# Optimization experiments

Measured on AMD Instinct MI355X. Metric: run time of the kernel, lower is better.

## Reference

```python
import jax, jax.numpy as jnp
import numpy as np

N_LAYERS = 4
D_MODEL = 64        # 8*8 hardcoded in source
D_STATE = 128
D_CONV = 4
EXPAND = 2
HEADDIM = 64        # Mamba2Simple default
D_INNER = EXPAND * D_MODEL            # 128
NHEADS = D_INNER // HEADDIM           # 2
NGROUPS = 1
D_IN_PROJ = 2 * D_INNER + 2 * NGROUPS * D_STATE + NHEADS   # 514
CONV_DIM = D_INNER + 2 * NGROUPS * D_STATE                 # 384
EPS = 1e-5
B_SZ, SEQ = 8, 4096


def setup_inputs() -> dict:
    key = jax.random.key(0)
    ks = jax.random.split(key, 8)
    s = 0.02
    x = jax.random.normal(ks[0], (B_SZ, SEQ, D_MODEL), jnp.float32)
    in_proj_w = jax.random.normal(ks[1], (N_LAYERS, D_IN_PROJ, D_MODEL), jnp.float32) * s
    conv_w = jax.random.normal(ks[2], (N_LAYERS, CONV_DIM, 1, D_CONV), jnp.float32) * 0.2
    conv_b = jnp.zeros((N_LAYERS, CONV_DIM), jnp.float32)
    # dt_bias ~ inverse-softplus of small dt values
    dt_bias = jax.random.uniform(ks[3], (N_LAYERS, NHEADS), jnp.float32, -4.0, 0.0)
    A_log = jnp.log(jax.random.uniform(ks[4], (N_LAYERS, NHEADS), jnp.float32, 1.0, 16.0))
    D = jnp.ones((N_LAYERS, NHEADS), jnp.float32)
    norm_w = jnp.ones((N_LAYERS, D_INNER), jnp.float32)
    out_proj_w = jax.random.normal(ks[5], (N_LAYERS, D_MODEL, D_INNER), jnp.float32) * s
    return {"x": x, "in_proj_w": in_proj_w, "conv_w": conv_w, "conv_b": conv_b,
            "dt_bias": dt_bias, "A_log": A_log, "D": D, "norm_w": norm_w,
            "out_proj_w": out_proj_w}


def _ssm(xh, dt, A, Bm, Cm):
    """Selective-scan SSM. xh:(B,L,H,P) dt:(B,L,H) A:(H,) Bm,Cm:(B,L,S) -> (B,L,H,P)"""
    dA = jnp.exp(dt * A)  # (B,L,H)

    def step(h, inp):
        dA_t, dt_t, x_t, B_t, C_t = inp
        # h: (B,H,P,S)
        h = h * dA_t[:, :, None, None] + (dt_t[:, :, None] * x_t)[..., None] * B_t[:, None, None, :]
        y = jnp.einsum('bhps,bs->bhp', h, C_t)
        return h, y

    b = xh.shape[0]
    h0 = jnp.zeros((b, NHEADS, HEADDIM, D_STATE), xh.dtype)
    xs = (jnp.moveaxis(dA, 1, 0), jnp.moveaxis(dt, 1, 0), jnp.moveaxis(xh, 1, 0),
          jnp.moveaxis(Bm, 1, 0), jnp.moveaxis(Cm, 1, 0))
    _, ys = jax.lax.scan(step, h0, xs)
    return jnp.moveaxis(ys, 0, 1)


def _layer(x, p):
    in_w, cw, cb, dtb, Alog, Dp, nw, ow = p
    zxbcdt = x @ in_w.T                                   # (B,L,514)
    z = zxbcdt[..., :D_INNER]
    xBC = zxbcdt[..., D_INNER:D_INNER + CONV_DIM]
    dt = jax.nn.softplus(zxbcdt[..., -NHEADS:] + dtb)     # (B,L,H)
    # causal depthwise conv over sequence
    xc = jnp.moveaxis(xBC, -1, 1)                         # (B,C,L)
    xc = jax.lax.conv_general_dilated(xc, cw, (1,), [(D_CONV - 1, 0)],
                                      dimension_numbers=('NCH', 'OIH', 'NCH'),
                                      feature_group_count=CONV_DIM)
    xBC = jax.nn.silu(jnp.moveaxis(xc + cb[None, :, None], 1, -1))
    xs = xBC[..., :D_INNER]
    Bm = xBC[..., D_INNER:D_INNER + D_STATE]
    Cm = xBC[..., D_INNER + D_STATE:]
    xh = xs.reshape(xs.shape[0], xs.shape[1], NHEADS, HEADDIM)
    A = -jnp.exp(Alog)                                    # (H,)
    y = _ssm(xh, dt, A, Bm, Cm) + Dp[None, None, :, None] * xh
    y = y.reshape(y.shape[0], y.shape[1], D_INNER)
    # gated RMSNorm (norm_before_gate=False): rmsnorm(y * silu(z)) * w
    y = y * jax.nn.silu(z)
    y = y * jax.lax.rsqrt(jnp.mean(y * y, axis=-1, keepdims=True) + EPS) * nw
    return y @ ow.T


def reference(x, in_proj_w, conv_w, conv_b, dt_bias, A_log, D, norm_w, out_proj_w):
    def body(xc, p):
        return _layer(xc, p) + xc, None
    out, _ = jax.lax.scan(body, x, (in_proj_w, conv_w, conv_b, dt_bias, A_log, D, norm_w, out_proj_w))
    return out
```

## Files before the change

kernel.cpp:

```cpp
#include <hip/hip_runtime.h>
#include <math.h>

#define B_SZ 8
#define SEQ  4096
#define DM   64
#define DI   128
#define NH   2
#define HD   64
#define DS   128
#define DIP  514
#define XW   384
#define CD   384
#define QC   64
#define NC   64
#define NR   (B_SZ*SEQ)
#define WPAD 576

typedef __attribute__((ext_vector_type(8))) short bf16x8;
typedef __attribute__((ext_vector_type(4))) float f32x4;
typedef __attribute__((ext_vector_type(2))) __bf16 bf16x2;

__device__ __forceinline__ unsigned short f2bf(float f) {
    union { __bf16 h; unsigned short u; } x;
    x.h = (__bf16)f;
    return x.u;
}
__device__ __forceinline__ unsigned int pk2(float lo, float hi) {
    union { bf16x2 v; unsigned int u; } x;
    x.v[0] = (__bf16)lo;
    x.v[1] = (__bf16)hi;
    return x.u;
}
__device__ __forceinline__ float bf2f(unsigned short h) {
    union { unsigned int u; float f; } x; x.u = ((unsigned int)h) << 16;
    return x.f;
}
__device__ __forceinline__ bf16x8 fragld(const unsigned short* base, int r0, int k0, int ld) {
    int l = threadIdx.x & 63;
    return *(const bf16x8*)(base + (ptrdiff_t)(r0 + (l & 15)) * ld + k0 + (l >> 4) * 8);
}

__global__ __launch_bounds__(256) void k_wcvt(const float* __restrict__ in_w,
                                              const float* __restrict__ out_w,
                                              unsigned short* __restrict__ Wb,
                                              unsigned short* __restrict__ OWb) {
    int idx = blockIdx.x * 256 + threadIdx.x;
    if (idx < 4 * WPAD * 64) {
        int l = idx / (WPAD * 64), r = idx % (WPAD * 64);
        int n = r >> 6, k = r & 63;
        float v = (n < DIP) ? in_w[(size_t)l * DIP * 64 + (size_t)n * 64 + k] : 0.f;
        Wb[idx] = f2bf(v);
    }
    if (idx < 4 * 64 * 128) OWb[idx] = f2bf(out_w[idx]);
}

__global__ __launch_bounds__(256) void k_xcvt(const float* __restrict__ X,
                                              unsigned short* __restrict__ Xb) {
    int idx = (blockIdx.x * 256 + threadIdx.x) * 4;
    float4 v = *(const float4*)(X + idx);
    uint2 p;
    p.x = pk2(v.x, v.y);
    p.y = pk2(v.z, v.w);
    *(uint2*)(Xb + idx) = p;
}

__global__ __launch_bounds__(256) void k_inproj(const unsigned short* __restrict__ Xb,
                                                const unsigned short* __restrict__ Wb,
                                                unsigned short* __restrict__ ZXb,
                                                float* __restrict__ DT) {
    int m0 = blockIdx.x * 256;
    int ny = blockIdx.y;
    int tid = threadIdx.x;
    int wid = tid >> 6, lane = tid & 63;
    int q4 = lane >> 4, c16 = lane & 15;
    int mb = m0 + wid * 64;
    bf16x8 af[4][2];
#pragma unroll
    for (int mt = 0; mt < 4; mt++)
#pragma unroll
        for (int ks = 0; ks < 2; ks++)
            af[mt][ks] = *(const bf16x8*)(Xb + (size_t)(mb + mt * 16 + c16) * 64 + ks * 32 + q4 * 8);
    if (ny < 6) {
#pragma unroll
        for (int nt = 0; nt < 4; nt++) {
            bf16x8 bf[2];
#pragma unroll
            for (int ks = 0; ks < 2; ks++)
                bf[ks] = *(const bf16x8*)(Wb + (size_t)(128 + ny * 64 + nt * 16 + c16) * 64 + ks * 32 + q4 * 8);
#pragma unroll
            for (int mt = 0; mt < 4; mt++) {
                f32x4 acc = {0.f, 0.f, 0.f, 0.f};
                acc = __builtin_amdgcn_mfma_f32_16x16x32_bf16(af[mt][0], bf[0], acc, 0, 0, 0);
                acc = __builtin_amdgcn_mfma_f32_16x16x32_bf16(af[mt][1], bf[1], acc, 0, 0, 0);
#pragma unroll
                for (int rr = 0; rr < 4; rr++) {
                    float v = acc[rr];
                    float vn = __shfl_xor(v, 1);
                    if (!(lane & 1)) {
                        unsigned int pk = pk2(v, vn);
                        *(unsigned int*)(ZXb + (size_t)(mb + mt * 16 + q4 * 4 + rr) * XW + ny * 64 + nt * 16 + c16) = pk;
                    }
                }
            }
        }
    } else {
        bf16x8 bf[2];
#pragma unroll
        for (int ks = 0; ks < 2; ks++)
            bf[ks] = *(const bf16x8*)(Wb + (size_t)(512 + c16) * 64 + ks * 32 + q4 * 8);
#pragma unroll
        for (int mt = 0; mt < 4; mt++) {
            f32x4 acc = {0.f, 0.f, 0.f, 0.f};
            acc = __builtin_amdgcn_mfma_f32_16x16x32_bf16(af[mt][0], bf[0], acc, 0, 0, 0);
            acc = __builtin_amdgcn_mfma_f32_16x16x32_bf16(af[mt][1], bf[1], acc, 0, 0, 0);
            if (c16 < 2)
#pragma unroll
                for (int rr = 0; rr < 4; rr++)
                    DT[(size_t)(mb + mt * 16 + q4 * 4 + rr) * 2 + c16] = acc[rr];
        }
    }
}

__global__ __launch_bounds__(1024, 8) void k_chunk1(
        const unsigned short* __restrict__ ZXb, const float* __restrict__ DT,
        const float* __restrict__ CW, const float* __restrict__ CB,
        const float* __restrict__ dtb, const float* __restrict__ Alog,
        const float* __restrict__ Dv,
        unsigned short* __restrict__ SL, unsigned short* __restrict__ CBuf,
        float* __restrict__ EB,
        float* __restrict__ TB, unsigned short* __restrict__ YBb) {
    __shared__ unsigned short sBt[128][72];
    __shared__ unsigned short sXt[128][72];
    __shared__ unsigned short uBC[2][64][136];
    __shared__ float s_cum[2][64], s_dt[2][64], s_w[2][64];
    unsigned short (*sM)[64][72] = (unsigned short (*)[64][72])&uBC[0][0][0];

    int c = blockIdx.x, b = blockIdx.y;
    size_t rbase = (size_t)b * SEQ + c * QC;
    int tid = threadIdx.x;
    int wid = tid >> 6, lane = tid & 63;
    int q4 = lane >> 4, c16 = lane & 15;

    if (wid < 2) {
        int h = wid, j = lane;
        float raw = DT[(rbase + j) * 2 + h] + dtb[h];
        float dt = (raw > 20.f) ? raw : log1pf(__expf(raw));
        float A = -__expf(Alog[h]);
        float x = dt * A;
        for (int off = 1; off < 64; off <<= 1) {
            float o = __shfl_up(x, off);
            if (lane >= off) x += o;
        }
        float T = __shfl(x, 63);
        s_dt[h][j] = dt;
        s_cum[h][j] = x;
        s_w[h][j] = __expf(T - x) * dt;
        EB[((size_t)(b * NC + c)) * 128 + h * 64 + j] = __expf(x);
        if (j == 0) TB[(b * 2 + h) * NC + c] = __expf(T);
    }

    size_t cbbase = ((size_t)(b * NC + c)) * 8192;
    for (int e = tid; e < 64 * 96; e += 1024) {
        int j = e / 96;
        int q = e - j * 96;
        int cc = q * 4;
        int l = c * QC + j;
        const unsigned short* zp = ZXb + (rbase + j) * XW + cc;
        uint2 a0 = *(const uint2*)zp;
        uint2 a1 = make_uint2(0, 0), a2 = make_uint2(0, 0), a3 = make_uint2(0, 0);
        if (l >= 1) a1 = *(const uint2*)(zp - XW);
        if (l >= 2) a2 = *(const uint2*)(zp - 2 * XW);
        if (l >= 3) a3 = *(const uint2*)(zp - 3 * XW);
        float v[4];
#pragma unroll
        for (int u = 0; u < 4; u++) {
            unsigned int w0 = (u < 2) ? a0.x : a0.y;
            unsigned int w1 = (u < 2) ? a1.x : a1.y;
            unsigned int w2 = (u < 2) ? a2.x : a2.y;
            unsigned int w3 = (u < 2) ? a3.x : a3.y;
            int sh = (u & 1) * 16;
            float r0 = bf2f((unsigned short)(w0 >> sh));
            float r1 = bf2f((unsigned short)(w1 >> sh));
            float r2 = bf2f((unsigned short)(w2 >> sh));
            float r3 = bf2f((unsigned short)(w3 >> sh));
            float4 wv = *(const float4*)(CW + (cc + u) * 4);
            float tt = CB[cc + u] + wv.w * r0 + wv.z * r1 + wv.y * r2 + wv.x * r3;
            v[u] = tt / (1.f + __expf(-tt));
        }
        if (cc < 128) {
#pragma unroll
            for (int u = 0; u < 4; u++) sXt[cc + u][j] = f2bf(v[u]);
        } else if (cc < 256) {
            int s = cc - 128;
            unsigned int p0 = pk2(v[0], v[1]);
            unsigned int p1 = pk2(v[2], v[3]);
            *(uint2*)&uBC[0][j][s] = make_uint2(p0, p1);
#pragma unroll
            for (int u = 0; u < 4; u++) sBt[s + u][j] = f2bf(v[u]);
        } else {
            int s = cc - 256;
            unsigned int p0 = pk2(v[0], v[1]);
            unsigned int p1 = pk2(v[2], v[3]);
            *(uint2*)&uBC[1][j][s] = make_uint2(p0, p1);
            *(uint2*)(CBuf + cbbase + (size_t)j * 128 + s) = make_uint2(p0, p1);
        }
    }
    __syncthreads();

    f32x4 gacc;
    {
        int it = wid >> 2, jt = wid & 3;
        f32x4 acc = {0.f, 0.f, 0.f, 0.f};
        for (int ks = 0; ks < 4; ks++) {
            bf16x8 a = fragld(&uBC[1][0][0], it * 16, ks * 32, 136);
            bf16x8 bb = fragld(&uBC[0][0][0], jt * 16, ks * 32, 136);
            acc = __builtin_amdgcn_mfma_f32_16x16x32_bf16(a, bb, acc, 0, 0, 0);
        }
        gacc = acc;
    }
    __syncthreads();
    {
        int it = wid >> 2, jt = wid & 3;
        int j = jt * 16 + c16;
        for (int rr = 0; rr < 4; rr++) {
            int i = it * 16 + q4 * 4 + rr;
            float gv = gacc[rr];
            for (int h = 0; h < 2; h++) {
                float m = 0.f;
                if (j <= i) m = gv * __expf(s_cum[h][i] - s_cum[h][j]) * s_dt[h][j];
                sM[h][i][j] = f2bf(m);
            }
        }
    }
    __syncthreads();

    size_t ybase = ((size_t)(b * NC + c)) * 8192;
#pragma unroll
    for (int u = 0; u < 2; u++) {
        int idx = wid * 2 + u;
        int h = idx >> 4, tt = idx & 15;
        int it = tt >> 2, pt = tt & 3;
        float dco = Dv[h];
        int pg = h * 64 + pt * 16 + c16;
        f32x4 acc;
        for (int rr = 0; rr < 4; rr++) {
            int i = it * 16 + q4 * 4 + rr;
            acc[rr] = dco * bf2f(sXt[pg][i]);
        }
        for (int ks = 0; ks < 2; ks++) {
            bf16x8 a = fragld(&sM[h][0][0], it * 16, ks * 32, 72);
            bf16x8 bb = fragld(&sXt[0][0], h * 64 + pt * 16, ks * 32, 72);
            acc = __builtin_amdgcn_mfma_f32_16x16x32_bf16(a, bb, acc, 0, 0, 0);
        }
        uint2 pk;
        pk.x = pk2(acc[0], acc[1]);
        pk.y = pk2(acc[2], acc[3]);
        *(uint2*)(YBb + ybase + (size_t)idx * 256 + lane * 4) = pk;
    }
    __syncthreads();
    {
        int row = tid >> 3, c0 = (tid & 7) * 8;
        uint4 xv = *(uint4*)&sXt[row][c0];
        const float* wp = s_w[row >> 6];
        unsigned int* px = &xv.x;
        uint4 ov;
        unsigned int* po = &ov.x;
#pragma unroll
        for (int t = 0; t < 4; t++) {
            float lo = bf2f((unsigned short)(px[t] & 0xffff)) * wp[c0 + 2 * t];
            float hi = bf2f((unsigned short)(px[t] >> 16)) * wp[c0 + 2 * t + 1];
            po[t] = pk2(lo, hi);
        }
        *(uint4*)&sXt[row][c0] = ov;
    }
    __syncthreads();
    size_t slbase = ((size_t)(b * NC + c)) * 16384;
#pragma unroll
    for (int u = 0; u < 4; u++) {
        int idx = wid * 4 + u;
        int ptl = idx >> 3, st = idx & 7;
        f32x4 acc = {0.f, 0.f, 0.f, 0.f};
        for (int ks = 0; ks < 2; ks++) {
            bf16x8 a = fragld(&sXt[0][0], ptl * 16, ks * 32, 72);
            bf16x8 bb = fragld(&sBt[0][0], st * 16, ks * 32, 72);
            acc = __builtin_amdgcn_mfma_f32_16x16x32_bf16(a, bb, acc, 0, 0, 0);
        }
        int s = st * 16 + c16;
        for (int rr = 0; rr < 4; rr++) {
            int p = ptl * 16 + q4 * 4 + rr;
            float vv = acc[rr];
            float vn = __shfl_xor(vv, 1);
            if (!(lane & 1)) {
                unsigned int pk = pk2(vv, vn);
                *(unsigned int*)(SL + slbase + (size_t)p * 128 + s) = pk;
            }
        }
    }
}

__global__ __launch_bounds__(256) void k_scan(unsigned short* __restrict__ SL,
                                              const float* __restrict__ TB) {
    int bid = blockIdx.x;
    int b = bid >> 5;
    int pu = (bid & 31) * 256 + threadIdx.x;
    int h = pu >> 12;
    const float* dAp = TB + (b * 2 + h) * NC;
    size_t base = (size_t)(b * NC) * 16384 + (size_t)pu * 2;
    float h0 = 0.f, h1 = 0.f;
#pragma unroll 8
    for (int cc = 0; cc < NC; cc++) {
        size_t idx = base + (size_t)cc * 16384;
        unsigned int v = *(unsigned int*)(SL + idx);
        float s0 = bf2f((unsigned short)(v & 0xffff));
        float s1 = bf2f((unsigned short)(v >> 16));
        *(unsigned int*)(SL + idx) = pk2(h0, h1);
        float dA = dAp[cc];
        h0 = h0 * dA + s0;
        h1 = h1 * dA + s1;
    }
}

__global__ __launch_bounds__(1024, 8) void k_fused(
        const unsigned short* __restrict__ SL, const unsigned short* __restrict__ CBuf,
        const float* __restrict__ EB,
        const unsigned short* __restrict__ YBb, const unsigned short* __restrict__ Wzb,
        const float* __restrict__ NW, const unsigned short* __restrict__ OWb,
        unsigned short* __restrict__ Xb, float* __restrict__ OutF,
        const unsigned short* __restrict__ WbN,
        unsigned short* __restrict__ ZXbO,
        float* __restrict__ DTO,
        int last) {
    __shared__ __attribute__((aligned(16))) unsigned short sH[128][136];
    __shared__ __attribute__((aligned(16))) unsigned short sE[128][136];
    float* sGf = (float*)&sH[0][0];
    unsigned short (*sG)[136] = (unsigned short (*)[136])&sE[0][0];
    unsigned short (*sX2)[72] = (unsigned short (*)[72])&sH[0][0];

    int c = blockIdx.x, b = blockIdx.y;
    size_t rbase = (size_t)b * SEQ + c * QC;
    int tid = threadIdx.x;
    int wid = tid >> 6, lane = tid & 63;
    size_t base = ((size_t)(b * NC + c)) * 16384;
    for (int u = 0; u < 2; u++) {
        int e = u * 1024 + tid;
        int row = e >> 4, cb8 = (e & 15) * 8;
        *(uint4*)&sH[row][cb8] = *(const uint4*)(SL + base + (size_t)row * 128 + cb8);
    }
    size_t cbbase = ((size_t)(b * NC + c)) * 8192;
    size_t ebase  = ((size_t)(b * NC + c)) * 128;
    {
        int i = tid >> 4, sc = (tid & 15) * 8;
        uint4 cv = *(const uint4*)(CBuf + cbbase + (size_t)i * 128 + sc);
        float e0 = EB[ebase + i], e1 = EB[ebase + 64 + i];
        unsigned int w[4] = {cv.x, cv.y, cv.z, cv.w};
        uint4 o0, o1;
        unsigned int* po0 = &o0.x;
        unsigned int* po1 = &o1.x;
#pragma unroll
        for (int t = 0; t < 4; t++) {
            float lo = bf2f((unsigned short)(w[t] & 0xffff));
            float hi = bf2f((unsigned short)(w[t] >> 16));
            po0[t] = pk2(lo * e0, hi * e0);
            po1[t] = pk2(lo * e1, hi * e1);
        }
        *(uint4*)&sE[i][sc] = o0;
        *(uint4*)&sE[64 + i][sc] = o1;
    }
    __syncthreads();
    int q4 = lane >> 4, c16 = lane & 15;

    float yv[2][4];
    int tit[2], tpg[2];
    size_t ybase = ((size_t)(b * NC + c)) * 8192;
#pragma unroll
    for (int u = 0; u < 2; u++) {
        int idx = wid * 2 + u;
        int h = idx >> 4, tt = idx & 15;
        int it = tt >> 2, pt = tt & 3;
        int pg = h * 64 + pt * 16 + c16;
        f32x4 zacc = {0.f, 0.f, 0.f, 0.f};
        f32x4 acc = {0.f, 0.f, 0.f, 0.f};
#pragma unroll
        for (int ks = 0; ks < 2; ks++) {
            bf16x8 xa = fragld(Xb, (int)rbase + it * 16, ks * 32, 64);
            bf16x8 wz = fragld(Wzb, h * 64 + pt * 16, ks * 32, 64);
            zacc = __builtin_amdgcn_mfma_f32_16x16x32_bf16(xa, wz, zacc, 0, 0, 0);
        }
        for (int ks = 0; ks < 4; ks++) {
            bf16x8 a = fragld(&sE[0][0], h * 64 + it * 16, ks * 32, 136);
            bf16x8 bb = fragld(&sH[0][0], h * 64 + pt * 16, ks * 32, 136);
            acc = __builtin_amdgcn_mfma_f32_16x16x32_bf16(a, bb, acc, 0, 0, 0);
        }
        tit[u] = it; tpg[u] = pg;
        uint2 yi = *(const uint2*)(YBb + ybase + (size_t)idx * 256 + lane * 4);
        float yin[4] = {bf2f((unsigned short)(yi.x & 0xffff)), bf2f((unsigned short)(yi.x >> 16)),
                        bf2f((unsigned short)(yi.y & 0xffff)), bf2f((unsigned short)(yi.y >> 16))};
        for (int rr = 0; rr < 4; rr++) {
            float y = acc[rr] + yin[rr];
            float z = zacc[rr];
            yv[u][rr] = y * (z / (1.f + __expf(-z)));
        }
    }
    __syncthreads();
#pragma unroll
    for (int u = 0; u < 2; u++)
        for (int rr = 0; rr < 4; rr++) {
            int i = tit[u] * 16 + q4 * 4 + rr;
            sGf[i * 132 + tpg[u]] = yv[u][rr];
        }
    __syncthreads();
    {
        int row = tid >> 4, part = tid & 15;
        int d0 = part * 8;
        float g[8];
        float ss = 0.f;
        for (int t2 = 0; t2 < 8; t2++) { g[t2] = sGf[row * 132 + d0 + t2]; ss += g[t2] * g[t2]; }
        ss += __shfl_xor(ss, 1);
        ss += __shfl_xor(ss, 2);
        ss += __shfl_xor(ss, 4);
        ss += __shfl_xor(ss, 8);
        float rms = rsqrtf(ss * (1.f / 128.f) + 1e-5f);
        for (int t2 = 0; t2 < 8; t2 += 2) {
            unsigned int pk = pk2(g[t2] * rms * NW[d0 + t2], g[t2 + 1] * rms * NW[d0 + t2 + 1]);
            *(unsigned int*)&sG[row][d0 + t2] = pk;
        }
    }
    __syncthreads();
    {
        int mt = wid >> 2, nt = wid & 3;
        f32x4 acc = {0.f, 0.f, 0.f, 0.f};
        for (int ks = 0; ks < 4; ks++) {
            bf16x8 a = fragld(&sG[0][0], mt * 16, ks * 32, 136);
            bf16x8 bb = *(const bf16x8*)(OWb + (size_t)(nt * 16 + c16) * 128 + ks * 32 + q4 * 8);
            acc = __builtin_amdgcn_mfma_f32_16x16x32_bf16(a, bb, acc, 0, 0, 0);
        }
        for (int rr = 0; rr < 4; rr++) {
            int m = mt * 16 + q4 * 4 + rr;
            int n = nt * 16 + c16;
            size_t o = (rbase + m) * DM + n;
            float v = bf2f(Xb[o]) + acc[rr];
            if (last) {
                OutF[o] = v;
            } else {
                unsigned short vb = f2bf(v);
                sX2[m][n] = vb;
                float vn = __shfl_xor(v, 1);
                if (!(lane & 1)) {
                    unsigned int pk = (unsigned int)vb | ((unsigned int)f2bf(vn) << 16);
                    *(unsigned int*)(Xb + o) = pk;
                }
            }
        }
    }
    if (!last) {
        __syncthreads();
        for (int t = wid; t < 100; t += 16) {
            int mt2, n0;
            int isdt = (t >= 96);
            if (!isdt) { mt2 = t & 3; n0 = (t >> 2) * 16; }
            else       { mt2 = t - 96; n0 = 0; }
            bf16x8 a0 = fragld(&sX2[0][0], mt2 * 16, 0, 72);
            bf16x8 a1 = fragld(&sX2[0][0], mt2 * 16, 32, 72);
            const unsigned short* wrow = isdt ? (WbN + (size_t)(512 + c16) * 64)
                                              : (WbN + (size_t)(128 + n0 + c16) * 64);
            bf16x8 b0 = *(const bf16x8*)(wrow + q4 * 8);
            bf16x8 b1 = *(const bf16x8*)(wrow + 32 + q4 * 8);
            f32x4 acc = {0.f, 0.f, 0.f, 0.f};
            acc = __builtin_amdgcn_mfma_f32_16x16x32_bf16(a0, b0, acc, 0, 0, 0);
            acc = __builtin_amdgcn_mfma_f32_16x16x32_bf16(a1, b1, acc, 0, 0, 0);
            if (!isdt) {
#pragma unroll
                for (int rr = 0; rr < 4; rr++) {
                    float v = acc[rr];
                    float vn = __shfl_xor(v, 1);
                    if (!(lane & 1)) {
                        unsigned int pk = pk2(v, vn);
                        *(unsigned int*)(ZXbO + (rbase + mt2 * 16 + q4 * 4 + rr) * XW + n0 + c16) = pk;
                    }
                }
            } else {
                if (c16 < 2)
#pragma unroll
                    for (int rr = 0; rr < 4; rr++)
                        DTO[(rbase + mt2 * 16 + q4 * 4 + rr) * 2 + c16] = acc[rr];
            }
        }
    }
}

extern "C" void kernel_launch(void* const* d_in, const int* in_sizes, int n_in,
                              void* d_out, int out_size, void* d_ws, size_t ws_size,
                              hipStream_t stream) {
    const float* x       = (const float*)d_in[0];
    const float* in_w    = (const float*)d_in[1];
    const float* conv_w  = (const float*)d_in[2];
    const float* conv_b  = (const float*)d_in[3];
    const float* dt_bias = (const float*)d_in[4];
    const float* A_log   = (const float*)d_in[5];
    const float* Dp      = (const float*)d_in[6];
    const float* norm_w  = (const float*)d_in[7];
    const float* out_w   = (const float*)d_in[8];
    float* out = (float*)d_out;
    float* ws  = (float*)d_ws;

    float* dt = ws;
    float* tb = dt + (size_t)NR * 2;
    float* eb = tb + 1024;
    unsigned short* zxb  = (unsigned short*)(eb + (size_t)B_SZ * NC * 128);
    unsigned short* ybb  = zxb + (size_t)NR * XW;
    unsigned short* sl   = ybb + (size_t)B_SZ * NC * 8192;
    unsigned short* cbuf = sl + (size_t)B_SZ * NC * 16384;
    unsigned short* xb   = cbuf + (size_t)B_SZ * NC * 8192;
    unsigned short* wb   = xb + (size_t)NR * DM;
    unsigned short* owb  = wb + (size_t)4 * WPAD * 64;

    k_wcvt<<<(4 * WPAD * 64 + 255) / 256, 256, 0, stream>>>(in_w, out_w, wb, owb);
    k_xcvt<<<NR * DM / 1024, 256, 0, stream>>>(x, xb);
    k_inproj<<<dim3(NR / 256, 7), 256, 0, stream>>>(xb, wb, zxb, dt);

    for (int layer = 0; layer < 4; layer++) {
        int nl = (layer < 3) ? layer + 1 : 3;
        k_chunk1<<<dim3(NC, B_SZ), 1024, 0, stream>>>(zxb, dt,
                conv_w + (size_t)layer * CD * 4, conv_b + (size_t)layer * CD,
                dt_bias + layer * NH, A_log + layer * NH, Dp + layer * NH,
                sl, cbuf, eb, tb, ybb);
        k_scan<<<256, 256, 0, stream>>>(sl, tb);
        k_fused<<<dim3(NC, B_SZ), 1024, 0, stream>>>(sl, cbuf, eb, ybb,
                wb + (size_t)layer * WPAD * 64, norm_w + layer * DI,
                owb + (size_t)layer * 64 * 128, xb, out,
                wb + (size_t)nl * WPAD * 64, zxb, dt,
                (layer == 3) ? 1 : 0);
    }
}
```

Baseline: 350.3 us.

## Recompute C and decay factors in fused kernel, parallelize inter-chunk scan

The chunk kernel no longer writes the C buffer or the per-row exp(cumsum) factors to global memory. The fused kernel now recomputes them from the in-projection output, redoing the conv, SiLU and dt prefix sum, and ping-pong buffers for zx/dt are added so the next layer's in-projection does not overwrite inputs still being read. The inter-chunk state scan is split into 8 segments per column with a shared-memory combine, which raises parallelism beyond the previous serial loop over 64 chunks. Weight and input conversion kernels are merged into one launch. The cost is extra recompute, more workspace, and an extra sync in the fused kernel.

```diff
diff --git a/kernel.cpp b/kernel.cpp
--- a/kernel.cpp
+++ b/kernel.cpp
@@ -40,28 +40,30 @@
     return *(const bf16x8*)(base + (ptrdiff_t)(r0 + (l & 15)) * ld + k0 + (l >> 4) * 8);
 }
 
-__global__ __launch_bounds__(256) void k_wcvt(const float* __restrict__ in_w,
-                                              const float* __restrict__ out_w,
-                                              unsigned short* __restrict__ Wb,
-                                              unsigned short* __restrict__ OWb) {
-    int idx = blockIdx.x * 256 + threadIdx.x;
-    if (idx < 4 * WPAD * 64) {
-        int l = idx / (WPAD * 64), r = idx % (WPAD * 64);
-        int n = r >> 6, k = r & 63;
-        float v = (n < DIP) ? in_w[(size_t)l * DIP * 64 + (size_t)n * 64 + k] : 0.f;
-        Wb[idx] = f2bf(v);
-    }
-    if (idx < 4 * 64 * 128) OWb[idx] = f2bf(out_w[idx]);
-}
-
-__global__ __launch_bounds__(256) void k_xcvt(const float* __restrict__ X,
-                                              unsigned short* __restrict__ Xb) {
-    int idx = (blockIdx.x * 256 + threadIdx.x) * 4;
-    float4 v = *(const float4*)(X + idx);
-    uint2 p;
-    p.x = pk2(v.x, v.y);
-    p.y = pk2(v.z, v.w);
-    *(uint2*)(Xb + idx) = p;
+__global__ __launch_bounds__(256) void k_pre(const float* __restrict__ in_w,
+                                             const float* __restrict__ out_w,
+                                             const float* __restrict__ X,
+                                             unsigned short* __restrict__ Wb,
+                                             unsigned short* __restrict__ OWb,
+                                             unsigned short* __restrict__ Xb) {
+    int bid = blockIdx.x;
+    if (bid < 576) {
+        int idx = bid * 256 + threadIdx.x;
+        if (idx < 4 * WPAD * 64) {
+            int l = idx / (WPAD * 64), r = idx % (WPAD * 64);
+            int n = r >> 6, k = r & 63;
+            float v = (n < DIP) ? in_w[(size_t)l * DIP * 64 + (size_t)n * 64 + k] : 0.f;
+            Wb[idx] = f2bf(v);
+        }
+        if (idx < 4 * 64 * 128) OWb[idx] = f2bf(out_w[idx]);
+    } else {
+        int idx = ((bid - 576) * 256 + threadIdx.x) * 4;
+        float4 v = *(const float4*)(X + idx);
+        uint2 p;
+        p.x = pk2(v.x, v.y);
+        p.y = pk2(v.z, v.w);
+        *(uint2*)(Xb + idx) = p;
+    }
 }
 
 __global__ __launch_bounds__(256) void k_inproj(const unsigned short* __restrict__ Xb,
@@ -126,8 +128,7 @@
         const float* __restrict__ CW, const float* __restrict__ CB,
         const float* __restrict__ dtb, const float* __restrict__ Alog,
         const float* __restrict__ Dv,
-        unsigned short* __restrict__ SL, unsigned short* __restrict__ CBuf,
-        float* __restrict__ EB,
+        unsigned short* __restrict__ SL,
         float* __restrict__ TB, unsigned short* __restrict__ YBb) {
     __shared__ unsigned short sBt[128][72];
     __shared__ unsigned short sXt[128][72];
@@ -155,11 +156,9 @@
         s_dt[h][j] = dt;
         s_cum[h][j] = x;
         s_w[h][j] = __expf(T - x) * dt;
-        EB[((size_t)(b * NC + c)) * 128 + h * 64 + j] = __expf(x);
         if (j == 0) TB[(b * 2 + h) * NC + c] = __expf(T);
     }
 
-    size_t cbbase = ((size_t)(b * NC + c)) * 8192;
     for (int e = tid; e < 64 * 96; e += 1024) {
         int j = e / 96;
         int q = e - j * 96;
@@ -202,7 +201,6 @@
             unsigned int p0 = pk2(v[0], v[1]);
             unsigned int p1 = pk2(v[2], v[3]);
             *(uint2*)&uBC[1][j][s] = make_uint2(p0, p1);
-            *(uint2*)(CBuf + cbbase + (size_t)j * 128 + s) = make_uint2(p0, p1);
         }
     }
     __syncthreads();
@@ -298,31 +296,56 @@
     }
 }
 
-__global__ __launch_bounds__(256) void k_scan(unsigned short* __restrict__ SL,
-                                              const float* __restrict__ TB) {
-    int bid = blockIdx.x;
-    int b = bid >> 5;
-    int pu = (bid & 31) * 256 + threadIdx.x;
-    int h = pu >> 12;
-    const float* dAp = TB + (b * 2 + h) * NC;
-    size_t base = (size_t)(b * NC) * 16384 + (size_t)pu * 2;
+__global__ __launch_bounds__(1024) void k_scan(unsigned short* __restrict__ SL,
+                                               const float* __restrict__ TB) {
+    __shared__ float sT0[8][128], sT1[8][128], sP[8];
+    int tid = threadIdx.x;
+    int col = tid & 127, seg = tid >> 7;
+    int colg = blockIdx.x * 128 + col;
+    int b2 = colg >> 13;
+    int pu = colg & 8191;
+    int h2 = pu >> 12;
+    const float* dAp = TB + (b2 * 2 + h2) * NC;
+    size_t cbase = (size_t)(b2 * NC) * 16384 + (size_t)pu * 2;
+    int cc0 = seg * 8;
+    unsigned int sv[8];
+    float dA[8];
+    float hP = 1.f, t0 = 0.f, t1 = 0.f;
+#pragma unroll
+    for (int k = 0; k < 8; k++) {
+        sv[k] = *(unsigned int*)(SL + cbase + (size_t)(cc0 + k) * 16384);
+        dA[k] = dAp[cc0 + k];
+        float sx0 = bf2f((unsigned short)(sv[k] & 0xffff));
+        float sx1 = bf2f((unsigned short)(sv[k] >> 16));
+        t0 = t0 * dA[k] + sx0;
+        t1 = t1 * dA[k] + sx1;
+        hP *= dA[k];
+    }
+    sT0[seg][col] = t0;
+    sT1[seg][col] = t1;
+    if (col == 0) sP[seg] = hP;
+    __syncthreads();
     float h0 = 0.f, h1 = 0.f;
-#pragma unroll 8
-    for (int cc = 0; cc < NC; cc++) {
-        size_t idx = base + (size_t)cc * 16384;
-        unsigned int v = *(unsigned int*)(SL + idx);
-        float s0 = bf2f((unsigned short)(v & 0xffff));
-        float s1 = bf2f((unsigned short)(v >> 16));
-        *(unsigned int*)(SL + idx) = pk2(h0, h1);
-        float dA = dAp[cc];
-        h0 = h0 * dA + s0;
-        h1 = h1 * dA + s1;
+    for (int s2 = 0; s2 < seg; s2++) {
+        float Ps = sP[s2];
+        h0 = h0 * Ps + sT0[s2][col];
+        h1 = h1 * Ps + sT1[s2][col];
+    }
+#pragma unroll
+    for (int k = 0; k < 8; k++) {
+        *(unsigned int*)(SL + cbase + (size_t)(cc0 + k) * 16384) = pk2(h0, h1);
+        float sx0 = bf2f((unsigned short)(sv[k] & 0xffff));
+        float sx1 = bf2f((unsigned short)(sv[k] >> 16));
+        h0 = h0 * dA[k] + sx0;
+        h1 = h1 * dA[k] + sx1;
     }
 }
 
 __global__ __launch_bounds__(1024, 8) void k_fused(
-        const unsigned short* __restrict__ SL, const unsigned short* __restrict__ CBuf,
-        const float* __restrict__ EB,
+        const unsigned short* __restrict__ SL, const float* __restrict__ DTin,
+        const unsigned short* __restrict__ ZXin,
+        const float* __restrict__ CW, const float* __restrict__ CB,
+        const float* __restrict__ dtb, const float* __restrict__ Alog,
         const unsigned short* __restrict__ YBb, const unsigned short* __restrict__ Wzb,
         const float* __restrict__ NW, const unsigned short* __restrict__ OWb,
         unsigned short* __restrict__ Xb, float* __restrict__ OutF,
@@ -332,6 +355,7 @@
         int last) {
     __shared__ __attribute__((aligned(16))) unsigned short sH[128][136];
     __shared__ __attribute__((aligned(16))) unsigned short sE[128][136];
+    __shared__ float s_e[2][64];
     float* sGf = (float*)&sH[0][0];
     unsigned short (*sG)[136] = (unsigned short (*)[136])&sE[0][0];
     unsigned short (*sX2)[72] = (unsigned short (*)[72])&sH[0][0];
@@ -341,30 +365,63 @@
     int tid = threadIdx.x;
     int wid = tid >> 6, lane = tid & 63;
     size_t base = ((size_t)(b * NC + c)) * 16384;
+
+    if (wid < 2) {
+        int h = wid, j = lane;
+        float raw = DTin[(rbase + j) * 2 + h] + dtb[h];
+        float dt = (raw > 20.f) ? raw : log1pf(__expf(raw));
+        float A = -__expf(Alog[h]);
+        float x = dt * A;
+        for (int off = 1; off < 64; off <<= 1) {
+            float o = __shfl_up(x, off);
+            if (lane >= off) x += o;
+        }
+        s_e[h][j] = __expf(x);
+    }
     for (int u = 0; u < 2; u++) {
         int e = u * 1024 + tid;
         int row = e >> 4, cb8 = (e & 15) * 8;
         *(uint4*)&sH[row][cb8] = *(const uint4*)(SL + base + (size_t)row * 128 + cb8);
     }
-    size_t cbbase = ((size_t)(b * NC + c)) * 8192;
-    size_t ebase  = ((size_t)(b * NC + c)) * 128;
+    __syncthreads();
     {
-        int i = tid >> 4, sc = (tid & 15) * 8;
-        uint4 cv = *(const uint4*)(CBuf + cbbase + (size_t)i * 128 + sc);
-        float e0 = EB[ebase + i], e1 = EB[ebase + 64 + i];
-        unsigned int w[4] = {cv.x, cv.y, cv.z, cv.w};
+        int j = tid >> 4, k8 = (tid & 15) * 8;
+        int l = c * QC + j;
+        const unsigned short* zp = ZXin + (rbase + j) * XW + 256 + k8;
+        uint4 a0 = *(const uint4*)zp;
+        uint4 a1 = make_uint4(0, 0, 0, 0), a2 = make_uint4(0, 0, 0, 0), a3 = make_uint4(0, 0, 0, 0);
+        if (l >= 1) a1 = *(const uint4*)(zp - XW);
+        if (l >= 2) a2 = *(const uint4*)(zp - 2 * XW);
+        if (l >= 3) a3 = *(const uint4*)(zp - 3 * XW);
+        float e0 = s_e[0][j], e1 = s_e[1][j];
+        const unsigned int* p0 = &a0.x;
+        const unsigned int* p1 = &a1.x;
+        const unsigned int* p2 = &a2.x;
+        const unsigned int* p3 = &a3.x;
         uint4 o0, o1;
-        unsigned int* po0 = &o0.x;
-        unsigned int* po1 = &o1.x;
+        unsigned int* q0 = &o0.x;
+        unsigned int* q1 = &o1.x;
 #pragma unroll
         for (int t = 0; t < 4; t++) {
-            float lo = bf2f((unsigned short)(w[t] & 0xffff));
-            float hi = bf2f((unsigned short)(w[t] >> 16));
-            po0[t] = pk2(lo * e0, hi * e0);
-            po1[t] = pk2(lo * e1, hi * e1);
-        }
-        *(uint4*)&sE[i][sc] = o0;
-        *(uint4*)&sE[64 + i][sc] = o1;
+            int ch = 256 + k8 + 2 * t;
+            float vv[2];
+#pragma unroll
+            for (int u = 0; u < 2; u++) {
+                int sh = u * 16;
+                float r0 = bf2f((unsigned short)(p0[t] >> sh));
+                float r1 = bf2f((unsigned short)(p1[t] >> sh));
+                float r2 = bf2f((unsigned short)(p2[t] >> sh));
+                float r3 = bf2f((unsigned short)(p3[t] >> sh));
+                float4 wv = *(const float4*)(CW + (ch + u) * 4);
+                float tt = CB[ch + u] + wv.w * r0 + wv.z * r1 + wv.y * r2 + wv.x * r3;
+                float v = tt / (1.f + __expf(-tt));
+                vv[u] = bf2f(f2bf(v));
+            }
+            q0[t] = pk2(vv[0] * e0, vv[1] * e0);
+            q1[t] = pk2(vv[0] * e1, vv[1] * e1);
+        }
+        *(uint4*)&sE[j][k8] = o0;
+        *(uint4*)&sE[64 + j][k8] = o1;
     }
     __syncthreads();
     int q4 = lane >> 4, c16 = lane & 15;
@@ -503,32 +560,37 @@
     float* out = (float*)d_out;
     float* ws  = (float*)d_ws;
 
-    float* dt = ws;
-    float* tb = dt + (size_t)NR * 2;
-    float* eb = tb + 1024;
-    unsigned short* zxb  = (unsigned short*)(eb + (size_t)B_SZ * NC * 128);
-    unsigned short* ybb  = zxb + (size_t)NR * XW;
+    float* dtA = ws;
+    float* dtB = dtA + (size_t)NR * 2;
+    float* tb  = dtB + (size_t)NR * 2;
+    unsigned short* zxbA = (unsigned short*)(tb + 1024);
+    unsigned short* zxbB = zxbA + (size_t)NR * XW;
+    unsigned short* ybb  = zxbB + (size_t)NR * XW;
     unsigned short* sl   = ybb + (size_t)B_SZ * NC * 8192;
-    unsigned short* cbuf = sl + (size_t)B_SZ * NC * 16384;
-    unsigned short* xb   = cbuf + (size_t)B_SZ * NC * 8192;
+    unsigned short* xb   = sl + (size_t)B_SZ * NC * 16384;
     unsigned short* wb   = xb + (size_t)NR * DM;
     unsigned short* owb  = wb + (size_t)4 * WPAD * 64;
 
-    k_wcvt<<<(4 * WPAD * 64 + 255) / 256, 256, 0, stream>>>(in_w, out_w, wb, owb);
-    k_xcvt<<<NR * DM / 1024, 256, 0, stream>>>(x, xb);
-    k_inproj<<<dim3(NR / 256, 7), 256, 0, stream>>>(xb, wb, zxb, dt);
+    k_pre<<<576 + NR * DM / 1024, 256, 0, stream>>>(in_w, out_w, x, wb, owb, xb);
+    k_inproj<<<dim3(NR / 256, 7), 256, 0, stream>>>(xb, wb, zxbA, dtA);
 
     for (int layer = 0; layer < 4; layer++) {
         int nl = (layer < 3) ? layer + 1 : 3;
-        k_chunk1<<<dim3(NC, B_SZ), 1024, 0, stream>>>(zxb, dt,
+        const unsigned short* zin = (layer & 1) ? zxbB : zxbA;
+        unsigned short* zout      = (layer & 1) ? zxbA : zxbB;
+        const float* din = (layer & 1) ? dtB : dtA;
+        float* dout      = (layer & 1) ? dtA : dtB;
+        k_chunk1<<<dim3(NC, B_SZ), 1024, 0, stream>>>(zin, din,
                 conv_w + (size_t)layer * CD * 4, conv_b + (size_t)layer * CD,
                 dt_bias + layer * NH, A_log + layer * NH, Dp + layer * NH,
-                sl, cbuf, eb, tb, ybb);
-        k_scan<<<256, 256, 0, stream>>>(sl, tb);
-        k_fused<<<dim3(NC, B_SZ), 1024, 0, stream>>>(sl, cbuf, eb, ybb,
-                wb + (size_t)layer * WPAD * 64, norm_w + layer * DI,
+                sl, tb, ybb);
+        k_scan<<<512, 1024, 0, stream>>>(sl, tb);
+        k_fused<<<dim3(NC, B_SZ), 1024, 0, stream>>>(sl, din, zin,
+                conv_w + (size_t)layer * CD * 4, conv_b + (size_t)layer * CD,
+                dt_bias + layer * NH, A_log + layer * NH,
+                ybb, wb + (size_t)layer * WPAD * 64, norm_w + layer * DI,
                 owb + (size_t)layer * 64 * 128, xb, out,
-                wb + (size_t)nl * WPAD * 64, zxb, dt,
+                wb + (size_t)nl * WPAD * 64, zout, dout,
                 (layer == 3) ? 1 : 0);
     }
 }
```

Measured after the change: 371.8 us. +6.1%, slower.
